# Performance work log

Hardware: AMD Instinct MI355X
Metric: run time of the kernel (lower is better)

Reference implementation:

```python
import jax, jax.numpy as jnp
import numpy as np

WINDOW = (8, 8)
NUM_HEADS = 6
PAD_H, PAD_W = WINDOW[0] // 2, WINDOW[1] // 2


def window_partition(x, wh, ww):
    # x: (B, C, H, W) -> (B*nh*nw, wh*ww, C)
    B, C, H, W = x.shape
    nh, nw = H // wh, W // ww
    x = x.reshape(B, C, nh, wh, nw, ww)
    x = x.transpose(0, 2, 4, 3, 5, 1)  # B, nh, nw, wh, ww, C
    return x.reshape(B * nh * nw, wh * ww, C)


def window_merge(x, B, C, H, W, wh, ww):
    # x: (B*nh*nw, wh*ww, C) -> (B, C, H, W)
    nh, nw = H // wh, W // ww
    x = x.reshape(B, nh, nw, wh, ww, C)
    x = x.transpose(0, 5, 1, 3, 2, 4)  # B, C, nh, wh, nw, ww
    return x.reshape(B, C, H, W)


def window_mha(t, num_heads):
    # t: (Bn, N, 3*C) packed qkv -> (Bn, N, C)
    Bn, N, C3 = t.shape
    C = C3 // 3
    d = C // num_heads
    q, k, v = jnp.split(t, 3, axis=-1)
    to_heads = lambda u: u.reshape(Bn, N, num_heads, d).transpose(0, 2, 1, 3)
    q, k, v = to_heads(q), to_heads(k), to_heads(v)
    scale = 1.0 / np.sqrt(d)
    attn = jax.nn.softmax(jnp.einsum('bhnd,bhmd->bhnm', q, k) * scale, axis=-1)
    o = jnp.einsum('bhnm,bhmd->bhnd', attn, v)
    return o.transpose(0, 2, 1, 3).reshape(Bn, N, C)


def setup_inputs() -> dict:
    key = jax.random.key(0)
    ks = jax.random.split(key, 5)
    B, C, H, W = 4, 384, 128, 128
    Cq = 64 * NUM_HEADS  # qkv_dim * num_heads = 384
    return {
        'x': jax.random.normal(ks[0], (B, C, H, W), dtype=jnp.float32),
        'w_qkv': jax.random.normal(ks[1], (3 * Cq, C), dtype=jnp.float32) * 0.02,
        'b_qkv': jax.random.normal(ks[2], (3 * Cq,), dtype=jnp.float32) * 0.02,
        'w_head': jax.random.normal(ks[3], (C, Cq), dtype=jnp.float32) * 0.02,
        'b_head': jax.random.normal(ks[4], (C,), dtype=jnp.float32) * 0.02,
    }


def reference(x, w_qkv, b_qkv, w_head, b_head):
    B, C, H, W = x.shape
    wh, ww = WINDOW
    # 1x1 conv qkv projection
    qkv = jnp.einsum('bchw,oc->bohw', x, w_qkv) + b_qkv[None, :, None, None]
    Cq = qkv.shape[1] // 3
    # branch 1: unpadded windows
    x1 = window_partition(qkv, wh, ww)
    x1 = window_mha(x1, NUM_HEADS)
    x1 = window_merge(x1, B, Cq, H, W, wh, ww)
    # branch 2: pad by half window, windows, then crop back
    qkv_p = jnp.pad(qkv, ((0, 0), (0, 0), (PAD_H, PAD_H), (PAD_W, PAD_W)))
    Hp, Wp = H + 2 * PAD_H, W + 2 * PAD_W
    x2 = window_partition(qkv_p, wh, ww)
    x2 = window_mha(x2, NUM_HEADS)
    x2 = window_merge(x2, B, Cq, Hp, Wp, wh, ww)
    x2 = x2[:, :, PAD_H:Hp - PAD_H, PAD_W:Wp - PAD_W]
    # merge + 1x1 conv head projection
    out = jnp.einsum('bchw,oc->bohw', x1 + x2, w_head) + b_head[None, :, None, None]
    return out
```

## Files before the change

kernel.cpp:

```cpp
#include <hip/hip_runtime.h>

typedef __bf16 bf16x8 __attribute__((ext_vector_type(8)));
typedef float f32x4 __attribute__((ext_vector_type(4)));

#define HW 16384
#define QKV_C 1152
#define SP 66

union U4B8 { uint4 u; bf16x8 v; __bf16 h[8]; };
union U2B4 { uint2 u; __bf16 h[4]; };

__global__ __launch_bounds__(256) void k_qkv(const float* __restrict__ x,
    const float* __restrict__ wq, const float* __restrict__ bq,
    __bf16* __restrict__ qkv)
{
    __shared__ __bf16 As[128 * 72];
    __shared__ __bf16 Bs[128 * 72];
    const int tid = threadIdx.x;
    const int hw0 = blockIdx.x * 128;
    const int o0  = blockIdx.y * 128;
    const int b   = blockIdx.z;
    const float* xb = x + (size_t)b * 384 * HW;

    f32x4 acc[4][4];
#pragma unroll
    for (int i = 0; i < 4; ++i)
#pragma unroll
        for (int j = 0; j < 4; ++j)
#pragma unroll
            for (int e = 0; e < 4; ++e) acc[i][j][e] = 0.0f;

    const int l = tid & 63;
    const int wv = tid >> 6;
    const int wm = wv & 1;
    const int wn = wv >> 1;
    const int l16 = l & 15, quad = l >> 4;

    for (int kt = 0; kt < 6; ++kt) {
        const int c0 = kt * 64;
#pragma unroll
        for (int it = 0; it < 8; ++it) {
            int unit = it * 256 + tid;
            int o = unit >> 4, ch = unit & 15;
            float4 f = *(const float4*)(wq + (size_t)(o0 + o) * 384 + c0 + ch * 4);
            U2B4 t;
            t.h[0] = (__bf16)f.x; t.h[1] = (__bf16)f.y;
            t.h[2] = (__bf16)f.z; t.h[3] = (__bf16)f.w;
            *(uint2*)(As + o * 72 + ch * 4) = t.u;
        }
#pragma unroll
        for (int ph = 0; ph < 4; ++ph) {
            int unit = ph * 256 + tid;
            int hw = unit & 127, c8 = unit >> 7;
            const float* xp = xb + (size_t)(c0 + c8 * 8) * HW + hw0 + hw;
            U4B8 t;
#pragma unroll
            for (int j = 0; j < 8; ++j) t.h[j] = (__bf16)xp[(size_t)j * HW];
            *(uint4*)(Bs + hw * 72 + c8 * 8) = t.u;
        }
        __syncthreads();
#pragma unroll
        for (int ks = 0; ks < 2; ++ks) {
            bf16x8 a[4], bb[4];
#pragma unroll
            for (int t = 0; t < 4; ++t)
                a[t] = *(const bf16x8*)(As + (wm * 64 + t * 16 + l16) * 72 + ks * 32 + quad * 8);
#pragma unroll
            for (int t = 0; t < 4; ++t)
                bb[t] = *(const bf16x8*)(Bs + (wn * 64 + t * 16 + l16) * 72 + ks * 32 + quad * 8);
#pragma unroll
            for (int mt = 0; mt < 4; ++mt)
#pragma unroll
                for (int nt = 0; nt < 4; ++nt)
                    acc[mt][nt] = __builtin_amdgcn_mfma_f32_16x16x32_bf16(
                        a[mt], bb[nt], acc[mt][nt], 0, 0, 0);
        }
        __syncthreads();
    }

    __bf16* qb = qkv + (size_t)b * HW * QKV_C;
#pragma unroll
    for (int mt = 0; mt < 4; ++mt) {
        int oo = o0 + wm * 64 + mt * 16 + quad * 4;
        float4 bias = *(const float4*)(bq + oo);
#pragma unroll
        for (int nt = 0; nt < 4; ++nt) {
            int hw = hw0 + wn * 64 + nt * 16 + l16;
            U2B4 t;
            t.h[0] = (__bf16)(acc[mt][nt][0] + bias.x);
            t.h[1] = (__bf16)(acc[mt][nt][1] + bias.y);
            t.h[2] = (__bf16)(acc[mt][nt][2] + bias.z);
            t.h[3] = (__bf16)(acc[mt][nt][3] + bias.w);
            *(uint2*)(qb + (size_t)hw * QKV_C + oo) = t.u;
        }
    }
}

__global__ __launch_bounds__(192) void k_attn(const __bf16* __restrict__ qkv,
    __bf16* __restrict__ y1, __bf16* __restrict__ y2)
{
    __shared__ __bf16 sm[3][2][64 * SP];
    const int tid = threadIdx.x;
    const int l = tid & 63, wv = tid >> 6;
    const int wid = blockIdx.x * 3 + wv;
    const bool shifted = wid >= 6144;
    const int w2 = shifted ? wid - 6144 : wid;
    const int head = w2 % 6;
    const int win = w2 / 6;
    const int nw = shifted ? 17 : 16;
    const int wx = win % nw;
    const int t2 = win / nw;
    const int wy = t2 % nw;
    const int b  = t2 / nw;
    const int h0 = wy * 8 - (shifted ? 4 : 0);
    const int w0 = wx * 8 - (shifted ? 4 : 0);
    const __bf16* qb = qkv + (size_t)b * HW * QKV_C;
    __bf16* VT = &sm[wv][0][0];
    __bf16* P  = &sm[wv][1][0];
    const int l16 = l & 15, quad = l >> 4;
    const int cbase = head * 64;

#pragma unroll
    for (int it = 0; it < 8; ++it) {
        int unit = it * 64 + l;
        int tok = unit >> 3, c8 = unit & 7;
        int hh = h0 + (tok >> 3), ww = w0 + (tok & 7);
        U4B8 t;
        if ((unsigned)hh < 128u && (unsigned)ww < 128u)
            t.u = *(const uint4*)(qb + (size_t)(hh * 128 + ww) * QKV_C + 768 + cbase + c8 * 8);
        else
            t.u = make_uint4(0, 0, 0, 0);
#pragma unroll
        for (int e = 0; e < 8; ++e) VT[(c8 * 8 + e) * SP + tok] = t.h[e];
    }

    size_t toff[4]; bool tval[4];
#pragma unroll
    for (int t = 0; t < 4; ++t) {
        int tok = t * 16 + l16;
        int hh = h0 + (tok >> 3), ww = w0 + (tok & 7);
        tval[t] = ((unsigned)hh < 128u && (unsigned)ww < 128u);
        toff[t] = tval[t] ? (size_t)(hh * 128 + ww) * QKV_C : 0;
    }

    f32x4 s[4][4];
#pragma unroll
    for (int i = 0; i < 4; ++i)
#pragma unroll
        for (int j = 0; j < 4; ++j)
#pragma unroll
            for (int e = 0; e < 4; ++e) s[i][j][e] = 0.0f;

#pragma unroll
    for (int ks = 0; ks < 2; ++ks) {
        bf16x8 aq[4], bk[4];
#pragma unroll
        for (int t = 0; t < 4; ++t) {
            U4B8 uq, uk;
            if (tval[t]) {
                uq.u = *(const uint4*)(qb + toff[t] + cbase + ks * 32 + quad * 8);
                uk.u = *(const uint4*)(qb + toff[t] + 384 + cbase + ks * 32 + quad * 8);
            } else {
                uq.u = make_uint4(0, 0, 0, 0);
                uk.u = make_uint4(0, 0, 0, 0);
            }
            aq[t] = uq.v;
            bk[t] = uk.v;
        }
#pragma unroll
        for (int mt = 0; mt < 4; ++mt)
#pragma unroll
            for (int nt = 0; nt < 4; ++nt)
                s[mt][nt] = __builtin_amdgcn_mfma_f32_16x16x32_bf16(
                    aq[mt], bk[nt], s[mt][nt], 0, 0, 0);
    }

#pragma unroll
    for (int mt = 0; mt < 4; ++mt) {
#pragma unroll
        for (int e = 0; e < 4; ++e) {
            float m_ = fmaxf(fmaxf(s[mt][0][e], s[mt][1][e]),
                             fmaxf(s[mt][2][e], s[mt][3][e]));
#pragma unroll
            for (int st = 1; st < 16; st <<= 1) m_ = fmaxf(m_, __shfl_xor(m_, st, 64));
            float p[4];
#pragma unroll
            for (int nt = 0; nt < 4; ++nt) p[nt] = __expf((s[mt][nt][e] - m_) * 0.125f);
            float sum = p[0] + p[1] + p[2] + p[3];
#pragma unroll
            for (int st = 1; st < 16; st <<= 1) sum += __shfl_xor(sum, st, 64);
            float r = __fdividef(1.0f, sum);
            int row = mt * 16 + quad * 4 + e;
#pragma unroll
            for (int nt = 0; nt < 4; ++nt)
                P[row * SP + nt * 16 + l16] = (__bf16)(p[nt] * r);
        }
    }
    __syncthreads();

    f32x4 o[4][4];
#pragma unroll
    for (int i = 0; i < 4; ++i)
#pragma unroll
        for (int j = 0; j < 4; ++j)
#pragma unroll
            for (int e = 0; e < 4; ++e) o[i][j][e] = 0.0f;

#pragma unroll
    for (int ks = 0; ks < 2; ++ks) {
        bf16x8 ap[4], bvv[4];
#pragma unroll
        for (int t = 0; t < 4; ++t)
            ap[t] = *(const bf16x8*)(P + (t * 16 + l16) * SP + ks * 32 + quad * 8);
#pragma unroll
        for (int t = 0; t < 4; ++t)
            bvv[t] = *(const bf16x8*)(VT + (t * 16 + l16) * SP + ks * 32 + quad * 8);
#pragma unroll
        for (int mt = 0; mt < 4; ++mt)
#pragma unroll
            for (int nt = 0; nt < 4; ++nt)
                o[mt][nt] = __builtin_amdgcn_mfma_f32_16x16x32_bf16(
                    ap[mt], bvv[nt], o[mt][nt], 0, 0, 0);
    }
    __syncthreads();

#pragma unroll
    for (int mt = 0; mt < 4; ++mt)
#pragma unroll
        for (int e = 0; e < 4; ++e) {
            int row = mt * 16 + quad * 4 + e;
#pragma unroll
            for (int nt = 0; nt < 4; ++nt)
                VT[row * SP + nt * 16 + l16] = (__bf16)o[mt][nt][e];
        }
    __syncthreads();

    __bf16* yb = (shifted ? y2 : y1) + (size_t)b * HW * 384;
#pragma unroll
    for (int it = 0; it < 8; ++it) {
        int unit = it * 64 + l;
        int tok = unit >> 3, c8 = unit & 7;
        int hh = h0 + (tok >> 3), ww = w0 + (tok & 7);
        if ((unsigned)hh < 128u && (unsigned)ww < 128u)
            *(uint4*)(yb + (size_t)(hh * 128 + ww) * 384 + cbase + c8 * 8) =
                *(const uint4*)(VT + tok * SP + c8 * 8);
    }
}

__global__ __launch_bounds__(256) void k_head(const __bf16* __restrict__ y1,
    const __bf16* __restrict__ y2, const float* __restrict__ wh,
    const float* __restrict__ bh, float* __restrict__ out)
{
    __shared__ __bf16 As[128 * 72];
    __shared__ __bf16 Bs[128 * 72];
    const int tid = threadIdx.x;
    const int hw0 = blockIdx.x * 128;
    const int o0  = blockIdx.y * 128;
    const int b   = blockIdx.z;
    const __bf16* y1b = y1 + (size_t)b * HW * 384;
    const __bf16* y2b = y2 + (size_t)b * HW * 384;

    f32x4 acc[4][4];
#pragma unroll
    for (int i = 0; i < 4; ++i)
#pragma unroll
        for (int j = 0; j < 4; ++j)
#pragma unroll
            for (int e = 0; e < 4; ++e) acc[i][j][e] = 0.0f;

    const int l = tid & 63, wv = tid >> 6;
    const int wm = wv & 1;
    const int wn = wv >> 1;
    const int l16 = l & 15, quad = l >> 4;

    for (int kt = 0; kt < 6; ++kt) {
        const int c0 = kt * 64;
#pragma unroll
        for (int it = 0; it < 4; ++it) {
            int unit = it * 256 + tid;
            int hw = unit >> 3, c8 = unit & 7;
            size_t off = (size_t)(hw0 + hw) * 384 + c0 + c8 * 8;
            U4B8 t1, t2, r;
            t1.u = *(const uint4*)(y1b + off);
            t2.u = *(const uint4*)(y2b + off);
#pragma unroll
            for (int e = 0; e < 8; ++e)
                r.h[e] = (__bf16)((float)t1.h[e] + (float)t2.h[e]);
            *(uint4*)(As + hw * 72 + c8 * 8) = r.u;
        }
#pragma unroll
        for (int it = 0; it < 8; ++it) {
            int unit = it * 256 + tid;
            int o = unit >> 4, ch = unit & 15;
            float4 f = *(const float4*)(wh + (size_t)(o0 + o) * 384 + c0 + ch * 4);
            U2B4 t;
            t.h[0] = (__bf16)f.x; t.h[1] = (__bf16)f.y;
            t.h[2] = (__bf16)f.z; t.h[3] = (__bf16)f.w;
            *(uint2*)(Bs + o * 72 + ch * 4) = t.u;
        }
        __syncthreads();
#pragma unroll
        for (int ks = 0; ks < 2; ++ks) {
            bf16x8 a[4], bb[4];
#pragma unroll
            for (int t = 0; t < 4; ++t)
                a[t] = *(const bf16x8*)(As + (wm * 64 + t * 16 + l16) * 72 + ks * 32 + quad * 8);
#pragma unroll
            for (int t = 0; t < 4; ++t)
                bb[t] = *(const bf16x8*)(Bs + (wn * 64 + t * 16 + l16) * 72 + ks * 32 + quad * 8);
#pragma unroll
            for (int mt = 0; mt < 4; ++mt)
#pragma unroll
                for (int nt = 0; nt < 4; ++nt)
                    acc[mt][nt] = __builtin_amdgcn_mfma_f32_16x16x32_bf16(
                        a[mt], bb[nt], acc[mt][nt], 0, 0, 0);
        }
        __syncthreads();
    }

#pragma unroll
    for (int nt = 0; nt < 4; ++nt) {
        int oo = o0 + wn * 64 + nt * 16 + l16;
        float bb_ = bh[oo];
        float* ob = out + ((size_t)b * 384 + oo) * HW + hw0 + wm * 64;
#pragma unroll
        for (int mt = 0; mt < 4; ++mt) {
            float4 f;
            f.x = acc[mt][nt][0] + bb_;
            f.y = acc[mt][nt][1] + bb_;
            f.z = acc[mt][nt][2] + bb_;
            f.w = acc[mt][nt][3] + bb_;
            *(float4*)(ob + mt * 16 + quad * 4) = f;
        }
    }
}

extern "C" void kernel_launch(void* const* d_in, const int* in_sizes, int n_in,
                              void* d_out, int out_size, void* d_ws, size_t ws_size,
                              hipStream_t stream) {
    const float* x  = (const float*)d_in[0];
    const float* wq = (const float*)d_in[1];
    const float* bq = (const float*)d_in[2];
    const float* wh = (const float*)d_in[3];
    const float* bh = (const float*)d_in[4];
    float* out = (float*)d_out;

    __bf16* qkv = (__bf16*)d_ws;
    __bf16* y1  = qkv + (size_t)4 * HW * QKV_C;
    __bf16* y2  = y1 + (size_t)4 * HW * 384;

    k_qkv<<<dim3(128, 9, 4), 256, 0, stream>>>(x, wq, bq, qkv);
    k_attn<<<dim3(4360), 192, 0, stream>>>(qkv, y1, y2);
    k_head<<<dim3(128, 3, 4), 256, 0, stream>>>(y1, y2, wh, bh, out);
}
```

Before: 495.6 us.

## Pre-transpose input to bf16 token-major and stage Q/K through LDS in attention

Adds a transpose kernel that converts x from channel-major fp32 into a token-major bf16 buffer (aliased onto y2), so the QKV GEMM loads its B tile with contiguous 16-byte reads. Previously every one of the nine output-channel blocks re-read and converted the strided fp32 input. The attention kernel now loads Q and K with coalesced per-token row loads into a padded LDS buffer and reads MFMA fragments from LDS instead of issuing scattered global loads. Weight loads are widened to 8 elements per thread. The cost is an extra kernel launch with its own global round trip, plus additional barriers and LDS traffic in attention.

```diff
diff --git a/kernel.cpp b/kernel.cpp
--- a/kernel.cpp
+++ b/kernel.cpp
@@ -5,12 +5,42 @@
 
 #define HW 16384
 #define QKV_C 1152
-#define SP 66
+#define SPV 66
+#define SPB 72
 
 union U4B8 { uint4 u; bf16x8 v; __bf16 h[8]; };
 union U2B4 { uint2 u; __bf16 h[4]; };
 
-__global__ __launch_bounds__(256) void k_qkv(const float* __restrict__ x,
+__global__ __launch_bounds__(256) void k_tr(const float* __restrict__ x,
+    __bf16* __restrict__ xT)
+{
+    __shared__ __bf16 T[64 * 72];
+    const int tid = threadIdx.x;
+    const int hw0 = blockIdx.x * 64;
+    const int c0  = blockIdx.y * 64;
+    const int b   = blockIdx.z;
+    const float* xb = x + ((size_t)b * 384 + c0) * HW + hw0;
+#pragma unroll
+    for (int ph = 0; ph < 2; ++ph) {
+        int unit = ph * 256 + tid;
+        int hw = unit & 63, c8 = unit >> 6;
+        const float* xp = xb + (size_t)(c8 * 8) * HW + hw;
+        U4B8 t;
+#pragma unroll
+        for (int j = 0; j < 8; ++j) t.h[j] = (__bf16)xp[(size_t)j * HW];
+        *(uint4*)(T + hw * 72 + c8 * 8) = t.u;
+    }
+    __syncthreads();
+    __bf16* ob = xT + ((size_t)b * HW + hw0) * 384 + c0;
+#pragma unroll
+    for (int ph = 0; ph < 2; ++ph) {
+        int unit = ph * 256 + tid;
+        int hw = unit >> 3, c8 = unit & 7;
+        *(uint4*)(ob + (size_t)hw * 384 + c8 * 8) = *(const uint4*)(T + hw * 72 + c8 * 8);
+    }
+}
+
+__global__ __launch_bounds__(256) void k_qkv(const __bf16* __restrict__ xT,
     const float* __restrict__ wq, const float* __restrict__ bq,
     __bf16* __restrict__ qkv)
 {
@@ -20,7 +50,7 @@
     const int hw0 = blockIdx.x * 128;
     const int o0  = blockIdx.y * 128;
     const int b   = blockIdx.z;
-    const float* xb = x + (size_t)b * 384 * HW;
+    const __bf16* xb = xT + (size_t)b * HW * 384;
 
     f32x4 acc[4][4];
 #pragma unroll
@@ -39,24 +69,25 @@
     for (int kt = 0; kt < 6; ++kt) {
         const int c0 = kt * 64;
 #pragma unroll
-        for (int it = 0; it < 8; ++it) {
+        for (int it = 0; it < 4; ++it) {
             int unit = it * 256 + tid;
-            int o = unit >> 4, ch = unit & 15;
-            float4 f = *(const float4*)(wq + (size_t)(o0 + o) * 384 + c0 + ch * 4);
-            U2B4 t;
-            t.h[0] = (__bf16)f.x; t.h[1] = (__bf16)f.y;
-            t.h[2] = (__bf16)f.z; t.h[3] = (__bf16)f.w;
-            *(uint2*)(As + o * 72 + ch * 4) = t.u;
-        }
-#pragma unroll
-        for (int ph = 0; ph < 4; ++ph) {
-            int unit = ph * 256 + tid;
-            int hw = unit & 127, c8 = unit >> 7;
-            const float* xp = xb + (size_t)(c0 + c8 * 8) * HW + hw0 + hw;
+            int o = unit >> 3, c8 = unit & 7;
+            const float* wp = wq + (size_t)(o0 + o) * 384 + c0 + c8 * 8;
+            float4 f0 = *(const float4*)(wp);
+            float4 f1 = *(const float4*)(wp + 4);
             U4B8 t;
-#pragma unroll
-            for (int j = 0; j < 8; ++j) t.h[j] = (__bf16)xp[(size_t)j * HW];
-            *(uint4*)(Bs + hw * 72 + c8 * 8) = t.u;
+            t.h[0] = (__bf16)f0.x; t.h[1] = (__bf16)f0.y;
+            t.h[2] = (__bf16)f0.z; t.h[3] = (__bf16)f0.w;
+            t.h[4] = (__bf16)f1.x; t.h[5] = (__bf16)f1.y;
+            t.h[6] = (__bf16)f1.z; t.h[7] = (__bf16)f1.w;
+            *(uint4*)(As + o * 72 + c8 * 8) = t.u;
+        }
+#pragma unroll
+        for (int it = 0; it < 4; ++it) {
+            int unit = it * 256 + tid;
+            int hw = unit >> 3, c8 = unit & 7;
+            *(uint4*)(Bs + hw * 72 + c8 * 8) =
+                *(const uint4*)(xb + (size_t)(hw0 + hw) * 384 + c0 + c8 * 8);
         }
         __syncthreads();
 #pragma unroll
@@ -99,7 +130,8 @@
 __global__ __launch_bounds__(192) void k_attn(const __bf16* __restrict__ qkv,
     __bf16* __restrict__ y1, __bf16* __restrict__ y2)
 {
-    __shared__ __bf16 sm[3][2][64 * SP];
+    __shared__ __bf16 smV[3][64 * SPV];
+    __shared__ __bf16 smB[3][64 * SPB];
     const int tid = threadIdx.x;
     const int l = tid & 63, wv = tid >> 6;
     const int wid = blockIdx.x * 3 + wv;
@@ -115,33 +147,55 @@
     const int h0 = wy * 8 - (shifted ? 4 : 0);
     const int w0 = wx * 8 - (shifted ? 4 : 0);
     const __bf16* qb = qkv + (size_t)b * HW * QKV_C;
-    __bf16* VT = &sm[wv][0][0];
-    __bf16* P  = &sm[wv][1][0];
+    __bf16* VT = smV[wv];
+    __bf16* BB = smB[wv];
     const int l16 = l & 15, quad = l >> 4;
     const int cbase = head * 64;
 
+    const int stok = l >> 3, sc8 = l & 7;
+    int soff[8];
 #pragma unroll
     for (int it = 0; it < 8; ++it) {
-        int unit = it * 64 + l;
-        int tok = unit >> 3, c8 = unit & 7;
+        int tok = it * 8 + stok;
         int hh = h0 + (tok >> 3), ww = w0 + (tok & 7);
+        soff[it] = ((unsigned)hh < 128u && (unsigned)ww < 128u)
+                 ? (hh * 128 + ww) * QKV_C + cbase + sc8 * 8 : -1;
+    }
+
+#pragma unroll
+    for (int it = 0; it < 8; ++it) {
+        int tok = it * 8 + stok;
         U4B8 t;
-        if ((unsigned)hh < 128u && (unsigned)ww < 128u)
-            t.u = *(const uint4*)(qb + (size_t)(hh * 128 + ww) * QKV_C + 768 + cbase + c8 * 8);
-        else
-            t.u = make_uint4(0, 0, 0, 0);
-#pragma unroll
-        for (int e = 0; e < 8; ++e) VT[(c8 * 8 + e) * SP + tok] = t.h[e];
-    }
-
-    size_t toff[4]; bool tval[4];
-#pragma unroll
-    for (int t = 0; t < 4; ++t) {
-        int tok = t * 16 + l16;
-        int hh = h0 + (tok >> 3), ww = w0 + (tok & 7);
-        tval[t] = ((unsigned)hh < 128u && (unsigned)ww < 128u);
-        toff[t] = tval[t] ? (size_t)(hh * 128 + ww) * QKV_C : 0;
-    }
+        if (soff[it] >= 0) t.u = *(const uint4*)(qb + soff[it] + 768);
+        else t.u = make_uint4(0, 0, 0, 0);
+#pragma unroll
+        for (int e = 0; e < 8; ++e) VT[(sc8 * 8 + e) * SPV + tok] = t.h[e];
+    }
+#pragma unroll
+    for (int it = 0; it < 8; ++it) {
+        int tok = it * 8 + stok;
+        U4B8 t;
+        if (soff[it] >= 0) t.u = *(const uint4*)(qb + soff[it]);
+        else t.u = make_uint4(0, 0, 0, 0);
+        *(uint4*)(BB + tok * SPB + sc8 * 8) = t.u;
+    }
+    __syncthreads();
+    bf16x8 aq[2][4];
+#pragma unroll
+    for (int ks = 0; ks < 2; ++ks)
+#pragma unroll
+        for (int t = 0; t < 4; ++t)
+            aq[ks][t] = *(const bf16x8*)(BB + (t * 16 + l16) * SPB + ks * 32 + quad * 8);
+    __syncthreads();
+#pragma unroll
+    for (int it = 0; it < 8; ++it) {
+        int tok = it * 8 + stok;
+        U4B8 t;
+        if (soff[it] >= 0) t.u = *(const uint4*)(qb + soff[it] + 384);
+        else t.u = make_uint4(0, 0, 0, 0);
+        *(uint4*)(BB + tok * SPB + sc8 * 8) = t.u;
+    }
+    __syncthreads();
 
     f32x4 s[4][4];
 #pragma unroll
@@ -150,31 +204,21 @@
         for (int j = 0; j < 4; ++j)
 #pragma unroll
             for (int e = 0; e < 4; ++e) s[i][j][e] = 0.0f;
-
 #pragma unroll
     for (int ks = 0; ks < 2; ++ks) {
-        bf16x8 aq[4], bk[4];
-#pragma unroll
-        for (int t = 0; t < 4; ++t) {
-            U4B8 uq, uk;
-            if (tval[t]) {
-                uq.u = *(const uint4*)(qb + toff[t] + cbase + ks * 32 + quad * 8);
-                uk.u = *(const uint4*)(qb + toff[t] + 384 + cbase + ks * 32 + quad * 8);
-            } else {
-                uq.u = make_uint4(0, 0, 0, 0);
-                uk.u = make_uint4(0, 0, 0, 0);
-            }
-            aq[t] = uq.v;
-            bk[t] = uk.v;
-        }
+        bf16x8 bk[4];
+#pragma unroll
+        for (int t = 0; t < 4; ++t)
+            bk[t] = *(const bf16x8*)(BB + (t * 16 + l16) * SPB + ks * 32 + quad * 8);
 #pragma unroll
         for (int mt = 0; mt < 4; ++mt)
 #pragma unroll
             for (int nt = 0; nt < 4; ++nt)
                 s[mt][nt] = __builtin_amdgcn_mfma_f32_16x16x32_bf16(
-                    aq[mt], bk[nt], s[mt][nt], 0, 0, 0);
-    }
-
+                    aq[ks][mt], bk[nt], s[mt][nt], 0, 0, 0);
+    }
+
+    float pr[4][4][4];
 #pragma unroll
     for (int mt = 0; mt < 4; ++mt) {
 #pragma unroll
@@ -190,12 +234,20 @@
 #pragma unroll
             for (int st = 1; st < 16; st <<= 1) sum += __shfl_xor(sum, st, 64);
             float r = __fdividef(1.0f, sum);
+#pragma unroll
+            for (int nt = 0; nt < 4; ++nt) pr[mt][nt][e] = p[nt] * r;
+        }
+    }
+    __syncthreads();
+#pragma unroll
+    for (int mt = 0; mt < 4; ++mt)
+#pragma unroll
+        for (int e = 0; e < 4; ++e) {
             int row = mt * 16 + quad * 4 + e;
 #pragma unroll
             for (int nt = 0; nt < 4; ++nt)
-                P[row * SP + nt * 16 + l16] = (__bf16)(p[nt] * r);
-        }
-    }
+                BB[row * SPB + nt * 16 + l16] = (__bf16)pr[mt][nt][e];
+        }
     __syncthreads();
 
     f32x4 o[4][4];
@@ -205,16 +257,15 @@
         for (int j = 0; j < 4; ++j)
 #pragma unroll
             for (int e = 0; e < 4; ++e) o[i][j][e] = 0.0f;
-
 #pragma unroll
     for (int ks = 0; ks < 2; ++ks) {
         bf16x8 ap[4], bvv[4];
 #pragma unroll
         for (int t = 0; t < 4; ++t)
-            ap[t] = *(const bf16x8*)(P + (t * 16 + l16) * SP + ks * 32 + quad * 8);
+            ap[t] = *(const bf16x8*)(BB + (t * 16 + l16) * SPB + ks * 32 + quad * 8);
 #pragma unroll
         for (int t = 0; t < 4; ++t)
-            bvv[t] = *(const bf16x8*)(VT + (t * 16 + l16) * SP + ks * 32 + quad * 8);
+            bvv[t] = *(const bf16x8*)(VT + (t * 16 + l16) * SPV + ks * 32 + quad * 8);
 #pragma unroll
         for (int mt = 0; mt < 4; ++mt)
 #pragma unroll
@@ -231,19 +282,19 @@
             int row = mt * 16 + quad * 4 + e;
 #pragma unroll
             for (int nt = 0; nt < 4; ++nt)
-                VT[row * SP + nt * 16 + l16] = (__bf16)o[mt][nt][e];
+                BB[row * SPB + nt * 16 + l16] = (__bf16)o[mt][nt][e];
         }
     __syncthreads();
 
     __bf16* yb = (shifted ? y2 : y1) + (size_t)b * HW * 384;
 #pragma unroll
     for (int it = 0; it < 8; ++it) {
-        int unit = it * 64 + l;
-        int tok = unit >> 3, c8 = unit & 7;
-        int hh = h0 + (tok >> 3), ww = w0 + (tok & 7);
-        if ((unsigned)hh < 128u && (unsigned)ww < 128u)
-            *(uint4*)(yb + (size_t)(hh * 128 + ww) * 384 + cbase + c8 * 8) =
-                *(const uint4*)(VT + tok * SP + c8 * 8);
+        int tok = it * 8 + stok;
+        if (soff[it] >= 0) {
+            int hh = h0 + (tok >> 3), ww = w0 + (tok & 7);
+            *(uint4*)(yb + (size_t)(hh * 128 + ww) * 384 + cbase + sc8 * 8) =
+                *(const uint4*)(BB + tok * SPB + sc8 * 8);
+        }
     }
 }
 
@@ -289,14 +340,18 @@
             *(uint4*)(As + hw * 72 + c8 * 8) = r.u;
         }
 #pragma unroll
-        for (int it = 0; it < 8; ++it) {
+        for (int it = 0; it < 4; ++it) {
             int unit = it * 256 + tid;
-            int o = unit >> 4, ch = unit & 15;
-            float4 f = *(const float4*)(wh + (size_t)(o0 + o) * 384 + c0 + ch * 4);
-            U2B4 t;
-            t.h[0] = (__bf16)f.x; t.h[1] = (__bf16)f.y;
-            t.h[2] = (__bf16)f.z; t.h[3] = (__bf16)f.w;
-            *(uint2*)(Bs + o * 72 + ch * 4) = t.u;
+            int o = unit >> 3, c8 = unit & 7;
+            const float* wp = wh + (size_t)(o0 + o) * 384 + c0 + c8 * 8;
+            float4 f0 = *(const float4*)(wp);
+            float4 f1 = *(const float4*)(wp + 4);
+            U4B8 t;
+            t.h[0] = (__bf16)f0.x; t.h[1] = (__bf16)f0.y;
+            t.h[2] = (__bf16)f0.z; t.h[3] = (__bf16)f0.w;
+            t.h[4] = (__bf16)f1.x; t.h[5] = (__bf16)f1.y;
+            t.h[6] = (__bf16)f1.z; t.h[7] = (__bf16)f1.w;
+            *(uint4*)(Bs + o * 72 + c8 * 8) = t.u;
         }
         __syncthreads();
 #pragma unroll
@@ -348,8 +403,10 @@
     __bf16* qkv = (__bf16*)d_ws;
     __bf16* y1  = qkv + (size_t)4 * HW * QKV_C;
     __bf16* y2  = y1 + (size_t)4 * HW * 384;
-
-    k_qkv<<<dim3(128, 9, 4), 256, 0, stream>>>(x, wq, bq, qkv);
+    __bf16* xT  = y2;
+
+    k_tr  <<<dim3(256, 6, 4), 256, 0, stream>>>(x, xT);
+    k_qkv <<<dim3(128, 9, 4), 256, 0, stream>>>(xT, wq, bq, qkv);
     k_attn<<<dim3(4360), 192, 0, stream>>>(qkv, y1, y2);
     k_head<<<dim3(128, 3, 4), 256, 0, stream>>>(y1, y2, wh, bh, out);
 }
```

Measured after the change: 501.5 us. About the same (+1.2%).
